# Performance work log

Measured on AMD Instinct MI355X. Metric: run time of the kernel, lower is better.

The kernel has to match this reference:

```python
import jax, jax.numpy as jnp
import numpy as np

B, D_IN, N_EXP, D_EXP, TOP_K = 8192, 1024, 8, 1024, 2


def setup_inputs() -> dict:
    key = jax.random.key(0)
    ks = jax.random.split(key, 6)
    s_in = 1.0 / np.sqrt(D_IN)
    s_exp = 1.0 / np.sqrt(D_EXP)
    return {
        "x": jax.random.normal(ks[0], (B, D_IN), jnp.float32),
        "gate_w": jax.random.normal(ks[1], (D_IN, N_EXP), jnp.float32) * s_in,
        "w1": jax.random.normal(ks[2], (N_EXP, D_IN, D_EXP), jnp.float32) * s_in,
        "b1": jax.random.normal(ks[3], (N_EXP, D_EXP), jnp.float32) * 0.01,
        "w2": jax.random.normal(ks[4], (N_EXP, D_EXP, D_EXP), jnp.float32) * s_exp,
        "b2": jax.random.normal(ks[5], (N_EXP, D_EXP), jnp.float32) * 0.01,
    }


def _moe(x, gate_w, w1, b1, w2, b2):
    # Gating: top-k sparse softmax over expert logits.
    gate_logits = x @ gate_w                          # (B, E)
    top_vals, top_idx = jax.lax.top_k(gate_logits, TOP_K)  # (B, K)
    # softmax over only the top-k logits == softmax of -inf-scattered logits
    top_w = jax.nn.softmax(top_vals, axis=-1)          # (B, K)
    gate_weights = jnp.zeros_like(gate_logits).at[
        jnp.arange(x.shape[0])[:, None], top_idx
    ].set(top_w)                                       # (B, E)
    # Dense all-expert MLP (matches torch.stack over experts).
    h = jax.nn.gelu(jnp.einsum("bd,edf->ebf", x, w1) + b1[:, None, :],
                    approximate=False)                 # (E, B, F)
    expert_outs = jnp.einsum("ebf,efg->ebg", h, w2) + b2[:, None, :]  # (E, B, G)
    output = jnp.einsum("be,ebg->bg", gate_weights, expert_outs)      # (B, G)
    return output, gate_weights


def reference(x, gate_w, w1, b1, w2, b2):
    return _moe(x, gate_w, w1, b1, w2, b2)
```

## Files before the change

kernel.cpp:

```cpp
#include <hip/hip_runtime.h>
#include <math.h>
#include <stdint.h>


#define NTOK   8192
#define DIN    1024
#define NEXP   8
#define DEXP   1024
#define MAXROWS 18432
#define MAXT   144

typedef __bf16 bf16x8_t __attribute__((ext_vector_type(8)));
typedef float f32x4 __attribute__((ext_vector_type(4)));

__device__ __forceinline__ unsigned short f2bf(float f) {
  union { float f; unsigned int u; } v; v.f = f;
  unsigned int u = v.u;
  u += 0x7fffu + ((u >> 16) & 1u);
  return (unsigned short)(u >> 16);
}

__device__ __forceinline__ float bf2f(unsigned short s) {
  union { unsigned int u; float f; } v; v.u = ((unsigned int)s) << 16;
  return v.f;
}

__device__ __forceinline__ void async16(const void* g, void* l) {
  __builtin_amdgcn_global_load_lds((const __attribute__((address_space(1))) void*)g,
                                   (__attribute__((address_space(3))) void*)l, 16, 0, 0);
}

__device__ __forceinline__ float gelu_fast(float v) {
  float u = v * (1.5957691216057308f + 0.07135481627f * v * v);
  return v * (1.0f / (1.0f + __expf(-u)));
}

__global__ __launch_bounds__(256) void gate_cast_kernel(const float* __restrict__ x,
                                                        const float* __restrict__ gw,
                                                        const float* __restrict__ w2,
                                                        unsigned short* __restrict__ xbf,
                                                        unsigned short* __restrict__ w2T,
                                                        float* __restrict__ outGate,
                                                        int* __restrict__ topE,
                                                        float* __restrict__ topW,
                                                        int* __restrict__ rowTok) {
  __shared__ __align__(16) char smem[32768];
  int b = blockIdx.x;
  int tid = threadIdx.x;
  if (b >= 4096) {
    int base = (b - 4096) * 1024 + tid * 4;
    *(int4*)(rowTok + base) = make_int4(-1, -1, -1, -1);
    return;
  }
  if (b >= 2048) {
    float* tile = (float*)smem;
    int idx = b - 2048;
    int e = idx >> 8, rest = idx & 255, kt = rest >> 4, nt = rest & 15;
    const float* s = w2 + (size_t)e * DEXP * DEXP + (size_t)kt * 64 * 1024 + nt * 64;
    unsigned short* d = w2T + (size_t)e * DEXP * DEXP + (size_t)nt * 64 * 1024 + kt * 64;
    int a = tid & 15, r0 = tid >> 4;
    #pragma unroll
    for (int p = 0; p < 4; ++p) {
      int r = r0 + p * 16;
      float4 v = *(const float4*)(s + (size_t)r * 1024 + a * 4);
      tile[r * 65 + a * 4 + 0] = v.x;
      tile[r * 65 + a * 4 + 1] = v.y;
      tile[r * 65 + a * 4 + 2] = v.z;
      tile[r * 65 + a * 4 + 3] = v.w;
    }
    __syncthreads();
    #pragma unroll
    for (int p = 0; p < 4; ++p) {
      int nr = r0 + p * 16;
      ushort4 o;
      o.x = f2bf(tile[(a * 4 + 0) * 65 + nr]);
      o.y = f2bf(tile[(a * 4 + 1) * 65 + nr]);
      o.z = f2bf(tile[(a * 4 + 2) * 65 + nr]);
      o.w = f2bf(tile[(a * 4 + 3) * 65 + nr]);
      *(ushort4*)(d + (size_t)nr * 1024 + a * 4) = o;
    }
    return;
  }
  float (*gwT)[1024] = (float(*)[1024])smem;
  #pragma unroll
  for (int it = 0; it < 8; ++it) {
    int idx = it * 256 + tid;
    int fk = idx >> 1;
    int e0 = (idx & 1) * 4;
    float4 g = *(const float4*)(gw + fk * 8 + e0);
    gwT[e0 + 0][fk] = g.x; gwT[e0 + 1][fk] = g.y;
    gwT[e0 + 2][fk] = g.z; gwT[e0 + 3][fk] = g.w;
  }
  __syncthreads();

  int lane = tid & 63, wv = tid >> 6;
  int t = b * 4 + wv;
  const float4* xr = (const float4*)(x + (size_t)t * 1024);
  ushort4* xo = (ushort4*)(xbf + (size_t)t * 1024);
  double acc[NEXP];
  #pragma unroll
  for (int e = 0; e < NEXP; ++e) acc[e] = 0.0;
  #pragma unroll
  for (int j = 0; j < 4; ++j) {
    int q = lane + 64 * j;
    float4 v = xr[q];
    ushort4 r;
    r.x = f2bf(v.x); r.y = f2bf(v.y); r.z = f2bf(v.z); r.w = f2bf(v.w);
    xo[q] = r;
    float vv[4] = {v.x, v.y, v.z, v.w};
    #pragma unroll
    for (int e = 0; e < NEXP; ++e) {
      float4 g = *(const float4*)&gwT[e][4 * q];
      acc[e] += (double)vv[0] * (double)g.x;
      acc[e] += (double)vv[1] * (double)g.y;
      acc[e] += (double)vv[2] * (double)g.z;
      acc[e] += (double)vv[3] * (double)g.w;
    }
  }
  #pragma unroll
  for (int off = 32; off > 0; off >>= 1) {
    #pragma unroll
    for (int e = 0; e < NEXP; ++e) acc[e] += __shfl_xor(acc[e], off);
  }
  if (lane == 0) {
    int e0 = 0; double v0 = acc[0];
    #pragma unroll
    for (int e = 1; e < NEXP; ++e) if (acc[e] > v0) { v0 = acc[e]; e0 = e; }
    int e1 = -1; double v1 = -1e300;
    #pragma unroll
    for (int e = 0; e < NEXP; ++e) if (e != e0 && acc[e] > v1) { v1 = acc[e]; e1 = e; }
    float ex = expf((float)(v1 - v0));
    float inv = 1.0f / (1.0f + ex);
    float w0 = inv, w1v = ex * inv;
    float g8[8];
    #pragma unroll
    for (int e = 0; e < NEXP; ++e) g8[e] = 0.f;
    g8[e0] = w0; g8[e1] = w1v;
    float4* gp = (float4*)(outGate + t * 8);
    gp[0] = *(float4*)&g8[0];
    gp[1] = *(float4*)&g8[4];
    topE[t * 2 + 0] = e0; topE[t * 2 + 1] = e1;
    topW[t * 2 + 0] = w0; topW[t * 2 + 1] = w1v;
  }
}

__global__ __launch_bounds__(1024) void slot_kernel(const int* __restrict__ topE,
                                                    int* __restrict__ topRow,
                                                    int* __restrict__ rowTok,
                                                    int* __restrict__ tileExpert,
                                                    int* __restrict__ tileRowBase,
                                                    const float* __restrict__ w1,
                                                    unsigned short* __restrict__ w1T) {
  __shared__ int wtot[16][NEXP];
  __shared__ int wbase[16][NEXP];
  __shared__ int soff[NEXP];
  __shared__ float tile[64 * 65];
  int tid = threadIdx.x;
  if (blockIdx.x != 0) {
    int idx = blockIdx.x - 1;
    int e = idx >> 8, rest = idx & 255, kt = rest >> 4, nt = rest & 15;
    const float* s = w1 + (size_t)e * DIN * DEXP + (size_t)kt * 64 * 1024 + nt * 64;
    unsigned short* d = w1T + (size_t)e * DIN * DEXP + (size_t)nt * 64 * 1024 + kt * 64;
    int a = tid & 15, r = tid >> 4;
    float4 v = *(const float4*)(s + (size_t)r * 1024 + a * 4);
    tile[r * 65 + a * 4 + 0] = v.x;
    tile[r * 65 + a * 4 + 1] = v.y;
    tile[r * 65 + a * 4 + 2] = v.z;
    tile[r * 65 + a * 4 + 3] = v.w;
    __syncthreads();
    int nr = r;
    ushort4 o;
    o.x = f2bf(tile[(a * 4 + 0) * 65 + nr]);
    o.y = f2bf(tile[(a * 4 + 1) * 65 + nr]);
    o.z = f2bf(tile[(a * 4 + 2) * 65 + nr]);
    o.w = f2bf(tile[(a * 4 + 3) * 65 + nr]);
    *(ushort4*)(d + (size_t)nr * 1024 + a * 4) = o;
    return;
  }
  int lane = tid & 63, wv = tid >> 6;
  int a0 = tid * 16;
  unsigned long long pk = 0ull;
  int cnt[NEXP];
  #pragma unroll
  for (int e = 0; e < NEXP; ++e) cnt[e] = 0;
  for (int i = 0; i < 16; ++i) {
    int e = topE[a0 + i];
    pk |= (unsigned long long)e << (i * 4);
    cnt[e]++;
  }
  int excl[NEXP];
  #pragma unroll
  for (int e = 0; e < NEXP; ++e) {
    int v = cnt[e], sum = v;
    #pragma unroll
    for (int d = 1; d < 64; d <<= 1) {
      int u = __shfl_up(sum, d);
      if (lane >= d) sum += u;
    }
    excl[e] = sum - v;
    if (lane == 63) wtot[wv][e] = sum;
  }
  __syncthreads();
  if (tid == 0) {
    int counts[NEXP];
    for (int e = 0; e < NEXP; ++e) {
      int s = 0;
      for (int w = 0; w < 16; ++w) { wbase[w][e] = s; s += wtot[w][e]; }
      counts[e] = s;
    }
    int row = 0, tl = 0;
    for (int e = 0; e < NEXP; ++e) {
      soff[e] = row;
      int nt256 = (counts[e] + 255) >> 8;
      for (int i = 0; i < nt256 * 2; ++i) {
        tileExpert[tl] = e; tileRowBase[tl] = row + i * 128; ++tl;
      }
      row += nt256 << 8;
    }
    for (; tl < MAXT; ++tl) tileExpert[tl] = -1;
  }
  __syncthreads();
  int base[NEXP], run[NEXP];
  #pragma unroll
  for (int e = 0; e < NEXP; ++e) { base[e] = soff[e] + wbase[wv][e] + excl[e]; run[e] = 0; }
  for (int i = 0; i < 16; ++i) {
    int e = (int)((pk >> (i * 4)) & 7ull);
    int row = base[e] + run[e]++;
    rowTok[row] = (a0 + i) >> 1;
    topRow[a0 + i] = row;
  }
}

template <bool GATHER, bool GELU>
__global__ __launch_bounds__(256, 4) void moe_gemm_kernel(
    const unsigned short* __restrict__ Asrc,
    const unsigned short* __restrict__ Wt,
    const float* __restrict__ bias,
    const int* __restrict__ tileExpert,
    const int* __restrict__ tileRowBase,
    const int* __restrict__ rowTok,
    unsigned short* __restrict__ Out) {
  int e = tileExpert[blockIdx.y];
  if (e < 0) return;
  int rowBase = tileRowBase[blockIdx.y];
  int n0 = blockIdx.x * 128;
  __shared__ __align__(16) unsigned short sm[16384];

  int tid = threadIdx.x;
  int lane = tid & 63, wv = tid >> 6;
  int wr = wv >> 1, wc = wv & 1;
  int rsel = lane & 15, q = (lane >> 4) & 3, rk = rsel & 3;
  int sr = tid >> 2;
  int swz = ((tid & 3) ^ (sr & 3)) * 8;

  int arow[2];
  #pragma unroll
  for (int j = 0; j < 2; ++j) {
    int r = rowBase + j * 64 + sr;
    if (GATHER) { int tk = rowTok[r]; arow[j] = tk < 0 ? 0 : tk; }
    else arow[j] = r;
  }
  const unsigned short* Bsrc = Wt + (size_t)e * 1024 * 1024;

  auto stage = [&](int T) {
    int kk = T * 32;
    int selB = (T & 1) * 16384;
    #pragma unroll
    for (int j = 0; j < 2; ++j) {
      int ab = __builtin_amdgcn_readfirstlane(selB + j * 4096 + wv * 1024);
      async16(Asrc + (size_t)arow[j] * 1024 + kk + swz, (char*)sm + ab);
      async16(Bsrc + (size_t)(n0 + j * 64 + sr) * 1024 + kk + swz,
              (char*)sm + ab + 8192);
    }
  };

  f32x4 acc[4][4] = {};

  stage(0);
  stage(1);
  asm volatile("s_waitcnt vmcnt(4)" ::: "memory");
  __builtin_amdgcn_s_barrier();

  for (int t = 0; t < 32; ++t) {
    const unsigned short* sA = sm + (t & 1) * 8192;
    const unsigned short* sB = sA + 4096;
    bf16x8_t af[4], bf[4];
    #pragma unroll
    for (int mi = 0; mi < 4; ++mi)
      af[mi] = *(const bf16x8_t*)&sA[(wr * 64 + mi * 16 + rsel) * 32 + (q ^ rk) * 8];
    #pragma unroll
    for (int ni = 0; ni < 4; ++ni)
      bf[ni] = *(const bf16x8_t*)&sB[(wc * 64 + ni * 16 + rsel) * 32 + (q ^ rk) * 8];
    __builtin_amdgcn_s_setprio(1);
    #pragma unroll
    for (int mi = 0; mi < 4; ++mi)
      #pragma unroll
      for (int ni = 0; ni < 4; ++ni)
        acc[mi][ni] = __builtin_amdgcn_mfma_f32_16x16x32_bf16(af[mi], bf[ni], acc[mi][ni], 0, 0, 0);
    __builtin_amdgcn_s_setprio(0);
    __builtin_amdgcn_s_barrier();
    if (t + 2 < 32) {
      stage(t + 2);
      asm volatile("s_waitcnt vmcnt(4)" ::: "memory");
    } else {
      asm volatile("s_waitcnt vmcnt(0)" ::: "memory");
    }
    __builtin_amdgcn_s_barrier();
  }

  float bv[4];
  int quad = lane >> 4;
  #pragma unroll
  for (int ni = 0; ni < 4; ++ni)
    bv[ni] = bias[e * 1024 + n0 + wc * 64 + ni * 16 + rsel];
  #pragma unroll
  for (int mi = 0; mi < 4; ++mi)
    #pragma unroll
    for (int ni = 0; ni < 4; ++ni)
      #pragma unroll
      for (int r = 0; r < 4; ++r) {
        int m = wr * 64 + mi * 16 + quad * 4 + r;
        int n = wc * 64 + ni * 16 + rsel;
        float v = acc[mi][ni][r] + bv[ni];
        if (GELU) v = gelu_fast(v);
        sm[m * 128 + n] = f2bf(v);
      }
  __syncthreads();
  #pragma unroll
  for (int i = 0; i < 8; ++i) {
    int idx = i * 4096 + tid * 16;
    int m = idx >> 8, cb = idx & 255;
    *(uint4*)(Out + (size_t)(rowBase + m) * 1024 + n0 + (cb >> 1)) =
        *(const uint4*)((const char*)sm + idx);
  }
}

__global__ __launch_bounds__(256) void combine_kernel(const unsigned short* __restrict__ y,
                                                      const int* __restrict__ topRow,
                                                      const float* __restrict__ topW,
                                                      float* __restrict__ out) {
  int tid = threadIdx.x;
  int wv = tid >> 6, lane = tid & 63;
  int t = blockIdx.x * 4 + wv;
  int r0 = topRow[t * 2 + 0], r1 = topRow[t * 2 + 1];
  float w0 = topW[t * 2 + 0], w1 = topW[t * 2 + 1];
  const unsigned short* p0 = y + (size_t)r0 * 1024 + lane * 16;
  const unsigned short* p1 = y + (size_t)r1 * 1024 + lane * 16;
  float* op = out + (size_t)t * 1024 + lane * 16;
  #pragma unroll
  for (int hh = 0; hh < 2; ++hh) {
    union { uint4 v; unsigned short s[8]; } a, b;
    a.v = *(const uint4*)(p0 + hh * 8);
    b.v = *(const uint4*)(p1 + hh * 8);
    float o[8];
    #pragma unroll
    for (int j = 0; j < 8; ++j)
      o[j] = w0 * bf2f(a.s[j]) + w1 * bf2f(b.s[j]);
    *(float4*)(op + hh * 8) = *(float4*)&o[0];
    *(float4*)(op + hh * 8 + 4) = *(float4*)&o[4];
  }
}

extern "C" void kernel_launch(void* const* d_in, const int* in_sizes, int n_in,
                              void* d_out, int out_size, void* d_ws, size_t ws_size,
                              hipStream_t stream) {
  const float* x  = (const float*)d_in[0];
  const float* gw = (const float*)d_in[1];
  const float* w1 = (const float*)d_in[2];
  const float* b1 = (const float*)d_in[3];
  const float* w2 = (const float*)d_in[4];
  const float* b2 = (const float*)d_in[5];
  float* out = (float*)d_out;

  char* ws = (char*)d_ws;
  int* tileExpert  = (int*)ws;
  int* tileRowBase = tileExpert + MAXT;
  int* topE        = tileRowBase + MAXT;
  int* topRow      = topE + 16384;
  float* topW      = (float*)(topRow + 16384);
  int* rowTok      = (int*)(ws + (256 << 10));
  unsigned short* xbf  = (unsigned short*)(ws + (512 << 10));
  unsigned short* w1T  = xbf + (size_t)NTOK * DIN;
  unsigned short* w2T  = w1T + (size_t)NEXP * DIN * DEXP;
  unsigned short* hbuf = w2T + (size_t)NEXP * DEXP * DEXP;
  unsigned short* ybuf = hbuf + (size_t)MAXROWS * DEXP;

  gate_cast_kernel<<<2048 + 2048 + 18, 256, 0, stream>>>(x, gw, w2, xbf, w2T,
                                                         out + (size_t)NTOK * DEXP,
                                                         topE, topW, rowTok);
  slot_kernel<<<1 + 2048, 1024, 0, stream>>>(topE, topRow, rowTok, tileExpert,
                                             tileRowBase, w1, w1T);
  moe_gemm_kernel<true, true><<<dim3(8, MAXT), 256, 0, stream>>>(
      xbf, w1T, b1, tileExpert, tileRowBase, rowTok, hbuf);
  moe_gemm_kernel<false, false><<<dim3(8, MAXT), 256, 0, stream>>>(
      hbuf, w2T, b2, tileExpert, tileRowBase, rowTok, ybuf);
  combine_kernel<<<NTOK / 4, 256, 0, stream>>>(ybuf, topRow, topW, out);
}
```

Baseline: 296.6 us.

## Pad experts to 128 rows, move w1 transpose to prep, reswizzle LDS layout

```diff
diff --git a/kernel.cpp b/kernel.cpp
--- a/kernel.cpp
+++ b/kernel.cpp
@@ -7,8 +7,8 @@
 #define DIN    1024
 #define NEXP   8
 #define DEXP   1024
-#define MAXROWS 18432
-#define MAXT   144
+#define MAXROWS 17408
+#define MAXT   136
 
 typedef __bf16 bf16x8_t __attribute__((ext_vector_type(8)));
 typedef float f32x4 __attribute__((ext_vector_type(4)));
@@ -35,50 +35,59 @@
   return v * (1.0f / (1.0f + __expf(-u)));
 }
 
-__global__ __launch_bounds__(256) void gate_cast_kernel(const float* __restrict__ x,
-                                                        const float* __restrict__ gw,
-                                                        const float* __restrict__ w2,
-                                                        unsigned short* __restrict__ xbf,
-                                                        unsigned short* __restrict__ w2T,
-                                                        float* __restrict__ outGate,
-                                                        int* __restrict__ topE,
-                                                        float* __restrict__ topW,
-                                                        int* __restrict__ rowTok) {
+__device__ __forceinline__ void transpose_tile(const float* s, unsigned short* d,
+                                               float* tile, int tid) {
+  int a = tid & 15, r0 = tid >> 4;
+  #pragma unroll
+  for (int p = 0; p < 4; ++p) {
+    int r = r0 + p * 16;
+    float4 v = *(const float4*)(s + (size_t)r * 1024 + a * 4);
+    tile[r * 65 + a * 4 + 0] = v.x;
+    tile[r * 65 + a * 4 + 1] = v.y;
+    tile[r * 65 + a * 4 + 2] = v.z;
+    tile[r * 65 + a * 4 + 3] = v.w;
+  }
+  __syncthreads();
+  #pragma unroll
+  for (int p = 0; p < 4; ++p) {
+    int nr = r0 + p * 16;
+    ushort4 o;
+    o.x = f2bf(tile[(a * 4 + 0) * 65 + nr]);
+    o.y = f2bf(tile[(a * 4 + 1) * 65 + nr]);
+    o.z = f2bf(tile[(a * 4 + 2) * 65 + nr]);
+    o.w = f2bf(tile[(a * 4 + 3) * 65 + nr]);
+    *(ushort4*)(d + (size_t)nr * 1024 + a * 4) = o;
+  }
+}
+
+__global__ __launch_bounds__(256) void prep_kernel(const float* __restrict__ x,
+                                                   const float* __restrict__ gw,
+                                                   const float* __restrict__ w1,
+                                                   const float* __restrict__ w2,
+                                                   unsigned short* __restrict__ xbf,
+                                                   unsigned short* __restrict__ w1T,
+                                                   unsigned short* __restrict__ w2T,
+                                                   float* __restrict__ outGate,
+                                                   int* __restrict__ topE,
+                                                   float* __restrict__ topW,
+                                                   int* __restrict__ rowTok) {
   __shared__ __align__(16) char smem[32768];
   int b = blockIdx.x;
   int tid = threadIdx.x;
-  if (b >= 4096) {
-    int base = (b - 4096) * 1024 + tid * 4;
+  if (b >= 6144) {
+    int base = (b - 6144) * 1024 + tid * 4;
     *(int4*)(rowTok + base) = make_int4(-1, -1, -1, -1);
     return;
   }
   if (b >= 2048) {
-    float* tile = (float*)smem;
     int idx = b - 2048;
+    const float* src = (idx < 2048) ? w1 : w2;
+    unsigned short* dst = (idx < 2048) ? w1T : w2T;
+    idx &= 2047;
     int e = idx >> 8, rest = idx & 255, kt = rest >> 4, nt = rest & 15;
-    const float* s = w2 + (size_t)e * DEXP * DEXP + (size_t)kt * 64 * 1024 + nt * 64;
-    unsigned short* d = w2T + (size_t)e * DEXP * DEXP + (size_t)nt * 64 * 1024 + kt * 64;
-    int a = tid & 15, r0 = tid >> 4;
-    #pragma unroll
-    for (int p = 0; p < 4; ++p) {
-      int r = r0 + p * 16;
-      float4 v = *(const float4*)(s + (size_t)r * 1024 + a * 4);
-      tile[r * 65 + a * 4 + 0] = v.x;
-      tile[r * 65 + a * 4 + 1] = v.y;
-      tile[r * 65 + a * 4 + 2] = v.z;
-      tile[r * 65 + a * 4 + 3] = v.w;
-    }
-    __syncthreads();
-    #pragma unroll
-    for (int p = 0; p < 4; ++p) {
-      int nr = r0 + p * 16;
-      ushort4 o;
-      o.x = f2bf(tile[(a * 4 + 0) * 65 + nr]);
-      o.y = f2bf(tile[(a * 4 + 1) * 65 + nr]);
-      o.z = f2bf(tile[(a * 4 + 2) * 65 + nr]);
-      o.w = f2bf(tile[(a * 4 + 3) * 65 + nr]);
-      *(ushort4*)(d + (size_t)nr * 1024 + a * 4) = o;
-    }
+    const float* s = src + (size_t)e * DIN * DEXP + (size_t)kt * 64 * 1024 + nt * 64;
+    unsigned short* d = dst + (size_t)e * DIN * DEXP + (size_t)nt * 64 * 1024 + kt * 64;
+    transpose_tile(s, d, (float*)smem, tid);
     return;
   }
   float (*gwT)[1024] = (float(*)[1024])smem;
@@ -148,45 +157,27 @@
                                                     int* __restrict__ topRow,
                                                     int* __restrict__ rowTok,
                                                     int* __restrict__ tileExpert,
-                                                    int* __restrict__ tileRowBase,
-                                                    const float* __restrict__ w1,
-                                                    unsigned short* __restrict__ w1T) {
+                                                    int* __restrict__ tileRowBase) {
   __shared__ int wtot[16][NEXP];
   __shared__ int wbase[16][NEXP];
   __shared__ int soff[NEXP];
-  __shared__ float tile[64 * 65];
   int tid = threadIdx.x;
-  if (blockIdx.x != 0) {
-    int idx = blockIdx.x - 1;
-    int e = idx >> 8, rest = idx & 255, kt = rest >> 4, nt = rest & 15;
-    const float* s = w1 + (size_t)e * DIN * DEXP + (size_t)kt * 64 * 1024 + nt * 64;
-    unsigned short* d = w1T + (size_t)e * DIN * DEXP + (size_t)nt * 64 * 1024 + kt * 64;
-    int a = tid & 15, r = tid >> 4;
-    float4 v = *(const float4*)(s + (size_t)r * 1024 + a * 4);
-    tile[r * 65 + a * 4 + 0] = v.x;
-    tile[r * 65 + a * 4 + 1] = v.y;
-    tile[r * 65 + a * 4 + 2] = v.z;
-    tile[r * 65 + a * 4 + 3] = v.w;
-    __syncthreads();
-    int nr = r;
-    ushort4 o;
-    o.x = f2bf(tile[(a * 4 + 0) * 65 + nr]);
-    o.y = f2bf(tile[(a * 4 + 1) * 65 + nr]);
-    o.z = f2bf(tile[(a * 4 + 2) * 65 + nr]);
-    o.w = f2bf(tile[(a * 4 + 3) * 65 + nr]);
-    *(ushort4*)(d + (size_t)nr * 1024 + a * 4) = o;
-    return;
-  }
   int lane = tid & 63, wv = tid >> 6;
   int a0 = tid * 16;
   unsigned long long pk = 0ull;
   int cnt[NEXP];
   #pragma unroll
   for (int e = 0; e < NEXP; ++e) cnt[e] = 0;
-  for (int i = 0; i < 16; ++i) {
-    int e = topE[a0 + i];
-    pk |= (unsigned long long)e << (i * 4);
-    cnt[e]++;
+  #pragma unroll
+  for (int i = 0; i < 4; ++i) {
+    int4 ev = *(const int4*)(topE + a0 + i * 4);
+    int e4[4] = {ev.x, ev.y, ev.z, ev.w};
+    #pragma unroll
+    for (int m = 0; m < 4; ++m) {
+      int e = e4[m];
+      pk |= (unsigned long long)e << ((i * 4 + m) * 4);
+      cnt[e]++;
+    }
   }
   int excl[NEXP];
   #pragma unroll
@@ -211,11 +202,9 @@
     int row = 0, tl = 0;
     for (int e = 0; e < NEXP; ++e) {
       soff[e] = row;
-      int nt256 = (counts[e] + 255) >> 8;
-      for (int i = 0; i < nt256 * 2; ++i) {
-        tileExpert[tl] = e; tileRowBase[tl] = row + i * 128; ++tl;
-      }
-      row += nt256 << 8;
+      int nt = (counts[e] + 127) >> 7;
+      for (int i = 0; i < nt; ++i) { tileExpert[tl] = e; tileRowBase[tl] = row + i * 128; ++tl; }
+      row += nt << 7;
     }
     for (; tl < MAXT; ++tl) tileExpert[tl] = -1;
   }
@@ -232,31 +221,37 @@
 }
 
 template <bool GATHER, bool GELU>
-__global__ __launch_bounds__(256, 4) void moe_gemm_kernel(
+__device__ __forceinline__ void moe_gemm_body(
     const unsigned short* __restrict__ Asrc,
     const unsigned short* __restrict__ Wt,
     const float* __restrict__ bias,
     const int* __restrict__ tileExpert,
     const int* __restrict__ tileRowBase,
     const int* __restrict__ rowTok,
-    unsigned short* __restrict__ Out) {
+    unsigned short* __restrict__ Out,
+    unsigned short* sm) {
   int e = tileExpert[blockIdx.y];
   if (e < 0) return;
   int rowBase = tileRowBase[blockIdx.y];
   int n0 = blockIdx.x * 128;
-  __shared__ __align__(16) unsigned short sm[16384];
 
   int tid = threadIdx.x;
   int lane = tid & 63, wv = tid >> 6;
   int wr = wv >> 1, wc = wv & 1;
-  int rsel = lane & 15, q = (lane >> 4) & 3, rk = rsel & 3;
-  int sr = tid >> 2;
-  int swz = ((tid & 3) ^ (sr & 3)) * 8;
+
+  int p = lane >> 3, pos = lane & 7;
+  int L = pos ^ p;
+  int rowoff = wv * 16 + p * 2 + (L >> 2);
+  int qsw = L & 3;
+
+  int rsel = lane & 15, quad = lane >> 4;
+  int prow = rsel >> 1;
+  int co = (((rsel & 1) * 4 + quad) ^ prow) * 8 + prow * 64;
 
   int arow[2];
   #pragma unroll
   for (int j = 0; j < 2; ++j) {
-    int r = rowBase + j * 64 + sr;
+    int r = rowBase + j * 64 + rowoff;
     if (GATHER) { int tk = rowTok[r]; arow[j] = tk < 0 ? 0 : tk; }
     else arow[j] = r;
   }
@@ -268,8 +263,8 @@
     #pragma unroll
     for (int j = 0; j < 2; ++j) {
       int ab = __builtin_amdgcn_readfirstlane(selB + j * 4096 + wv * 1024);
-      async16(Asrc + (size_t)arow[j] * 1024 + kk + swz, (char*)sm + ab);
-      async16(Bsrc + (size_t)(n0 + j * 64 + sr) * 1024 + kk + swz,
+      async16(Asrc + (size_t)arow[j] * 1024 + kk + qsw * 8, (char*)sm + ab);
+      async16(Bsrc + (size_t)(n0 + j * 64 + rowoff) * 1024 + kk + qsw * 8,
               (char*)sm + ab + 8192);
     }
   };
@@ -287,10 +282,10 @@
     bf16x8_t af[4], bf[4];
     #pragma unroll
     for (int mi = 0; mi < 4; ++mi)
-      af[mi] = *(const bf16x8_t*)&sA[(wr * 64 + mi * 16 + rsel) * 32 + (q ^ rk) * 8];
+      af[mi] = *(const bf16x8_t*)&sA[wr * 2048 + mi * 512 + co];
     #pragma unroll
     for (int ni = 0; ni < 4; ++ni)
-      bf[ni] = *(const bf16x8_t*)&sB[(wc * 64 + ni * 16 + rsel) * 32 + (q ^ rk) * 8];
+      bf[ni] = *(const bf16x8_t*)&sB[wc * 2048 + ni * 512 + co];
     __builtin_amdgcn_s_setprio(1);
     #pragma unroll
     for (int mi = 0; mi < 4; ++mi)
@@ -309,7 +304,6 @@
   }
 
   float bv[4];
-  int quad = lane >> 4;
   #pragma unroll
   for (int ni = 0; ni < 4; ++ni)
     bv[ni] = bias[e * 1024 + n0 + wc * 64 + ni * 16 + rsel];
@@ -333,6 +327,24 @@
     *(uint4*)(Out + (size_t)(rowBase + m) * 1024 + n0 + (cb >> 1)) =
         *(const uint4*)((const char*)sm + idx);
   }
+}
+
+__global__ __launch_bounds__(256, 4) void gemm1_kernel(
+    const unsigned short* __restrict__ xbf, const unsigned short* __restrict__ w1T,
+    const float* __restrict__ b1, const int* __restrict__ tileExpert,
+    const int* __restrict__ tileRowBase, const int* __restrict__ rowTok,
+    unsigned short* __restrict__ h) {
+  __shared__ __align__(16) unsigned short sm[16384];
+  moe_gemm_body<true, true>(xbf, w1T, b1, tileExpert, tileRowBase, rowTok, h, sm);
+}
+
+__global__ __launch_bounds__(256, 4) void gemm2_kernel(
+    const unsigned short* __restrict__ h, const unsigned short* __restrict__ w2T,
+    const float* __restrict__ b2, const int* __restrict__ tileExpert,
+    const int* __restrict__ tileRowBase, const int* __restrict__ rowTok,
+    unsigned short* __restrict__ y) {
+  __shared__ __align__(16) unsigned short sm[16384];
+  moe_gemm_body<false, false>(h, w2T, b2, tileExpert, tileRowBase, rowTok, y, sm);
 }
 
 __global__ __launch_bounds__(256) void combine_kernel(const unsigned short* __restrict__ y,
@@ -385,14 +397,13 @@
   unsigned short* hbuf = w2T + (size_t)NEXP * DEXP * DEXP;
   unsigned short* ybuf = hbuf + (size_t)MAXROWS * DEXP;
 
-  gate_cast_kernel<<<2048 + 2048 + 18, 256, 0, stream>>>(x, gw, w2, xbf, w2T,
-                                                         out + (size_t)NTOK * DEXP,
-                                                         topE, topW, rowTok);
-  slot_kernel<<<1 + 2048, 1024, 0, stream>>>(topE, topRow, rowTok, tileExpert,
-                                             tileRowBase, w1, w1T);
-  moe_gemm_kernel<true, true><<<dim3(8, MAXT), 256, 0, stream>>>(
-      xbf, w1T, b1, tileExpert, tileRowBase, rowTok, hbuf);
-  moe_gemm_kernel<false, false><<<dim3(8, MAXT), 256, 0, stream>>>(
-      hbuf, w2T, b2, tileExpert, tileRowBase, rowTok, ybuf);
+  prep_kernel<<<2048 + 4096 + 17, 256, 0, stream>>>(x, gw, w1, w2, xbf, w1T, w2T,
+                                                    out + (size_t)NTOK * DEXP,
+                                                    topE, topW, rowTok);
+  slot_kernel<<<1, 1024, 0, stream>>>(topE, topRow, rowTok, tileExpert, tileRowBase);
+  gemm1_kernel<<<dim3(8, MAXT), 256, 0, stream>>>(xbf, w1T, b1, tileExpert,
+                                                  tileRowBase, rowTok, hbuf);
+  gemm2_kernel<<<dim3(8, MAXT), 256, 0, stream>>>(hbuf, w2T, b2, tileExpert,
+                                                  tileRowBase, rowTok, ybuf);
   combine_kernel<<<NTOK / 4, 256, 0, stream>>>(ybuf, topRow, topW, out);
 }
```

Result: slower. 303.6 us (+2.4%).
